# Optimization experiments

Measured on AMD Instinct MI355X. Metric: run time of the kernel, lower is better.

The kernel has to match this reference:

```python
import jax, jax.numpy as jnp
import numpy as np

N_NODES = 50000
N_EDGES = 800000
NODE_IN = 128
EDGE_IN = 16
HIDDEN = 128
OUT = 128


def setup_inputs() -> dict:
    key = jax.random.key(0)
    ks = jax.random.split(key, 8)
    x = jax.random.normal(ks[0], (N_NODES, NODE_IN), dtype=jnp.float32)
    edge_index = jax.random.randint(ks[1], (2, N_EDGES), 0, N_NODES, dtype=jnp.int64)
    edge_attr = jax.random.normal(ks[2], (N_EDGES, EDGE_IN), dtype=jnp.float32)
    # Linear weights stored as [in, out] (torch Linear weight is [out, in]); kaiming-ish scale
    s1 = 1.0 / np.sqrt(NODE_IN + EDGE_IN)
    s2 = 1.0 / np.sqrt(HIDDEN + EDGE_IN)
    W1 = jax.random.uniform(ks[3], (NODE_IN + EDGE_IN, HIDDEN), jnp.float32, -s1, s1)
    b1 = jnp.zeros((HIDDEN,), jnp.float32)
    W2 = jax.random.uniform(ks[4], (HIDDEN + EDGE_IN, OUT), jnp.float32, -s2, s2)
    b2 = jnp.zeros((OUT,), jnp.float32)
    return {"x": x, "edge_index": edge_index, "edge_attr": edge_attr,
            "W1": W1, "b1": b1, "W2": W2, "b2": b2}


def _edge_conv(x, src, dst, edge_attr, W, b, num_nodes):
    # message: lin(cat([x_j, edge_attr])) == x_j @ W_x + edge_attr @ W_e
    d = x.shape[1]
    Wx, We = W[:d], W[d:]
    msg = x[src] @ Wx + edge_attr @ We           # [E, out]
    aggr = jax.ops.segment_sum(msg, dst, num_segments=num_nodes)  # scatter-add
    return aggr + b


def reference(x, edge_index, edge_attr, W1, b1, W2, b2):
    src, dst = edge_index[0], edge_index[1]
    h = jax.nn.relu(_edge_conv(x, src, dst, edge_attr, W1, b1, N_NODES))
    return _edge_conv(h, src, dst, edge_attr, W2, b2, N_NODES)
```

## Files before the change

kernel.cpp:

```cpp
#include <hip/hip_runtime.h>

#define N_NODES 50000
#define N_EDGES 800000
#define F_NODE 128
#define F_EDGE 16

#define BUCK_SH 6
#define NBUCK ((N_NODES + 63) >> BUCK_SH)
#define NPART 8
#define CAP_PART 304
#define BCUR_STRIDE 16

#define CONV_BLOCKS ((N_NODES * 32 + 255) / 256)
#define SCAT_BLOCKS ((N_EDGES + 255) / 256)
#define NB128 ((N_NODES + 3) / 4)
#define NB16  ((N_NODES + 3) / 4)

__device__ __forceinline__ unsigned int bf16_rn(float f) {
    unsigned int u = __float_as_uint(f);
    unsigned int r = ((u >> 16) & 1u) + 0x7fffu;
    return (u + r) >> 16;
}
__device__ __forceinline__ unsigned int pack_bf16(float a, float b) {
    return bf16_rn(a) | (bf16_rn(b) << 16);
}
__device__ __forceinline__ float bf_lo(unsigned int u) { return __uint_as_float(u << 16); }
__device__ __forceinline__ float bf_hi(unsigned int u) { return __uint_as_float(u & 0xffff0000u); }

__global__ __launch_bounds__(256) void convert_and_scatter(
    const float4* __restrict__ x4, uint2* __restrict__ xb2,
    const int* __restrict__ src, const int* __restrict__ dst,
    int* __restrict__ bcur, unsigned long long* __restrict__ temp)
{
    if (blockIdx.x < CONV_BLOCKS) {
        int i = blockIdx.x * 256 + threadIdx.x;
        float4 v = x4[i];
        uint2 o;
        o.x = pack_bf16(v.x, v.y);
        o.y = pack_bf16(v.z, v.w);
        xb2[i] = o;
    } else {
        int e = (int)(blockIdx.x - CONV_BLOCKS) * 256 + threadIdx.x;
        if (e >= N_EDGES) return;
        int d = dst[e];
        int b = d >> BUCK_SH;
        int dl = d & 63;
        int cell = b * NPART + (blockIdx.x & (NPART - 1));
        int pos = atomicAdd(&bcur[cell * BCUR_STRIDE], 1);
        if (pos < CAP_PART)
            temp[(size_t)cell * CAP_PART + pos] =
                (unsigned long long)src[e] |
                ((unsigned long long)e  << 17) |
                ((unsigned long long)dl << 37);
    }
}

__global__ __launch_bounds__(1024) void cell_scan(const int* __restrict__ bcur,
                                                  int* __restrict__ bucket_base) {
    __shared__ int sh[1024];
    int t = threadIdx.x;
    int tot = 0;
    if (t < NBUCK) {
        #pragma unroll
        for (int p = 0; p < NPART; ++p) {
            int m = bcur[(t * NPART + p) * BCUR_STRIDE];
            tot += (m > CAP_PART ? CAP_PART : m);
        }
    }
    sh[t] = tot;
    __syncthreads();
    for (int off = 1; off < 1024; off <<= 1) {
        int v = (t >= off) ? sh[t - off] : 0;
        __syncthreads();
        sh[t] += v;
        __syncthreads();
    }
    if (t < NBUCK) bucket_base[t] = sh[t] - tot;
}

__global__ __launch_bounds__(256) void bucket_permute(
    const unsigned long long* __restrict__ temp,
    const int* __restrict__ bcur,
    const int* __restrict__ bucket_base,
    int* __restrict__ rs,
    int* __restrict__ csr_src, int* __restrict__ csr_eid)
{
    __shared__ int cnt[64];
    __shared__ int scn[64];
    __shared__ int cnt2[64];
    int b = blockIdx.x;
    int tid = threadIdx.x;
    int node0 = b << BUCK_SH;
    int nn = min(64, N_NODES - node0);
    if (tid < 64) { cnt[tid] = 0; cnt2[tid] = 0; }
    __syncthreads();
    int base = bucket_base[b];

    for (int part = 0; part < NPART; ++part) {
        int cell = b * NPART + part;
        int m = bcur[cell * BCUR_STRIDE];
        if (m > CAP_PART) m = CAP_PART;
        size_t tb = (size_t)cell * CAP_PART;
        for (int i = tid; i < m; i += 256) {
            int dl = (int)(temp[tb + i] >> 37);
            atomicAdd(&cnt[dl], 1);
        }
    }
    __syncthreads();

    if (tid < 64) scn[tid] = cnt[tid];
    __syncthreads();
    for (int o = 1; o < 64; o <<= 1) {
        int v = 0;
        if (tid < 64 && tid >= o) v = scn[tid - o];
        __syncthreads();
        if (tid < 64) scn[tid] += v;
        __syncthreads();
    }
    if (tid < nn) rs[node0 + tid] = base + scn[tid] - cnt[tid];
    if (b == NBUCK - 1 && tid == 0) rs[N_NODES] = base + scn[63];

    for (int part = 0; part < NPART; ++part) {
        int cell = b * NPART + part;
        int m = bcur[cell * BCUR_STRIDE];
        if (m > CAP_PART) m = CAP_PART;
        size_t tb = (size_t)cell * CAP_PART;
        for (int i = tid; i < m; i += 256) {
            unsigned long long v = temp[tb + i];
            int s  = (int)(v & 0x1FFFF);
            int ei = (int)((v >> 17) & 0xFFFFF);
            int dl = (int)(v >> 37);
            int pos = base + (scn[dl] - cnt[dl]) + atomicAdd(&cnt2[dl], 1);
            csr_src[pos] = s;
            csr_eid[pos] = ei;
        }
    }
}

__device__ __forceinline__ void agg128_body(const unsigned int* __restrict__ xb,
                                            const int* __restrict__ rs,
                                            const int* __restrict__ csr_src,
                                            float* __restrict__ xa,
                                            int bid) {
    int gid = bid * 256 + (int)threadIdx.x;
    int n = gid >> 6;
    int lane = threadIdx.x & 63;
    if (n >= N_NODES) return;
    int beg = rs[n], end = rs[n + 1];
    float a0 = 0.f, a1 = 0.f;
    int i = beg;
    for (; i + 8 <= end; i += 8) {
        int s[8];
        #pragma unroll
        for (int t = 0; t < 8; ++t) s[t] = csr_src[i + t];
        unsigned int u[8];
        #pragma unroll
        for (int t = 0; t < 8; ++t) u[t] = xb[(size_t)s[t] * 64 + lane];
        #pragma unroll
        for (int t = 0; t < 8; ++t) { a0 += bf_lo(u[t]); a1 += bf_hi(u[t]); }
    }
    for (; i + 4 <= end; i += 4) {
        int s[4];
        #pragma unroll
        for (int t = 0; t < 4; ++t) s[t] = csr_src[i + t];
        unsigned int u[4];
        #pragma unroll
        for (int t = 0; t < 4; ++t) u[t] = xb[(size_t)s[t] * 64 + lane];
        #pragma unroll
        for (int t = 0; t < 4; ++t) { a0 += bf_lo(u[t]); a1 += bf_hi(u[t]); }
    }
    for (; i < end; ++i) {
        unsigned int u = xb[(size_t)csr_src[i] * 64 + lane];
        a0 += bf_lo(u);
        a1 += bf_hi(u);
    }
    *(float2*)(xa + (size_t)n * F_NODE + lane * 2) = make_float2(a0, a1);
}

__device__ __forceinline__ void agg16_body(const float4* __restrict__ eattr4,
                                           const int* __restrict__ rs,
                                           const int* __restrict__ csr_eid,
                                           float* __restrict__ eagg,
                                           int bid) {
    int gid = bid * 256 + (int)threadIdx.x;
    int n = gid >> 6;
    int lane = threadIdx.x & 63;
    int sub = lane >> 2;
    int j4  = lane & 3;
    if (n >= N_NODES) return;
    int beg = rs[n], end = rs[n + 1];
    float4 acc = make_float4(0.f, 0.f, 0.f, 0.f);
    for (int i = beg + sub; i < end; i += 16) {
        int eid = csr_eid[i];
        float4 v = eattr4[(size_t)eid * 4 + j4];
        acc.x += v.x; acc.y += v.y; acc.z += v.z; acc.w += v.w;
    }
    #pragma unroll
    for (int m = 4; m <= 32; m <<= 1) {
        acc.x += __shfl_xor(acc.x, m, 64);
        acc.y += __shfl_xor(acc.y, m, 64);
        acc.z += __shfl_xor(acc.z, m, 64);
        acc.w += __shfl_xor(acc.w, m, 64);
    }
    if (sub == 0) *(float4*)(eagg + (size_t)n * F_EDGE + j4 * 4) = acc;
}

__global__ __launch_bounds__(256) void agg_combo(const unsigned int* __restrict__ xb,
                                                 const float4* __restrict__ eattr4,
                                                 const int* __restrict__ rs,
                                                 const int* __restrict__ csr_src,
                                                 const int* __restrict__ csr_eid,
                                                 float* __restrict__ xa,
                                                 float* __restrict__ eagg) {
    if (blockIdx.x < NB128)
        agg128_body(xb, rs, csr_src, xa, blockIdx.x);
    else
        agg16_body(eattr4, rs, csr_eid, eagg, blockIdx.x - NB128);
}

__global__ __launch_bounds__(256) void agg128_bf16(const unsigned int* __restrict__ xb,
                                                   const int* __restrict__ rs,
                                                   const int* __restrict__ csr_src,
                                                   float* __restrict__ xa) {
    agg128_body(xb, rs, csr_src, xa, blockIdx.x);
}

#define BM 64
#define BK 16
#define LDA (BM + 4)
#define LDB (128 + 4)

__global__ __launch_bounds__(256) void layer_gemm(
    const float* xa,
    const float* __restrict__ eagg,
    const float* __restrict__ W,
    const float* __restrict__ bias,
    float* out_f32,
    unsigned int* __restrict__ out_bf,
    int do_relu, int out_bf16)
{
    __shared__ float As[BK][LDA];
    __shared__ float Bs[BK][LDB];
    const int tid = threadIdx.x;
    const int bm = blockIdx.x * BM;

    const int tcol = (tid & 15) * 8;
    const int trow = (tid >> 4) * 4;

    const int lm = tid >> 2;
    const int lk = (tid & 3) * 4;
    const int bk = tid >> 4;
    const int bj = (tid & 15) * 8;

    const int row = bm + lm;
    const bool rowok = row < N_NODES;

    float acc[4][8];
    #pragma unroll
    for (int i = 0; i < 4; ++i)
        #pragma unroll
        for (int j = 0; j < 8; ++j) acc[i][j] = 0.f;

    for (int k0 = 0; k0 < 144; k0 += BK) {
        float4 av = make_float4(0.f, 0.f, 0.f, 0.f);
        if (rowok) {
            if (k0 < F_NODE)
                av = *(const float4*)(xa + (size_t)row * F_NODE + k0 + lk);
            else
                av = *(const float4*)(eagg + (size_t)row * F_EDGE + lk);
        }
        As[lk + 0][lm] = av.x;
        As[lk + 1][lm] = av.y;
        As[lk + 2][lm] = av.z;
        As[lk + 3][lm] = av.w;

        const float4 b0 = *(const float4*)(W + (size_t)(k0 + bk) * 128 + bj);
        const float4 b1 = *(const float4*)(W + (size_t)(k0 + bk) * 128 + bj + 4);
        *(float4*)(&Bs[bk][bj])     = b0;
        *(float4*)(&Bs[bk][bj + 4]) = b1;
        __syncthreads();

        #pragma unroll
        for (int k = 0; k < BK; ++k) {
            float a0 = As[k][trow + 0];
            float a1 = As[k][trow + 1];
            float a2 = As[k][trow + 2];
            float a3 = As[k][trow + 3];
            float bv[8];
            #pragma unroll
            for (int j = 0; j < 8; ++j) bv[j] = Bs[k][tcol + j];
            #pragma unroll
            for (int j = 0; j < 8; ++j) {
                acc[0][j] = fmaf(a0, bv[j], acc[0][j]);
                acc[1][j] = fmaf(a1, bv[j], acc[1][j]);
                acc[2][j] = fmaf(a2, bv[j], acc[2][j]);
                acc[3][j] = fmaf(a3, bv[j], acc[3][j]);
            }
        }
        __syncthreads();
    }

    float4 bb0 = *(const float4*)(bias + tcol);
    float4 bb1 = *(const float4*)(bias + tcol + 4);
    #pragma unroll
    for (int i = 0; i < 4; ++i) {
        int r = bm + trow + i;
        if (r >= N_NODES) break;
        float v[8];
        v[0] = acc[i][0] + bb0.x; v[1] = acc[i][1] + bb0.y;
        v[2] = acc[i][2] + bb0.z; v[3] = acc[i][3] + bb0.w;
        v[4] = acc[i][4] + bb1.x; v[5] = acc[i][5] + bb1.y;
        v[6] = acc[i][6] + bb1.z; v[7] = acc[i][7] + bb1.w;
        if (do_relu) {
            #pragma unroll
            for (int j = 0; j < 8; ++j) v[j] = fmaxf(v[j], 0.f);
        }
        if (out_bf16) {
            uint4 s;
            s.x = pack_bf16(v[0], v[1]);
            s.y = pack_bf16(v[2], v[3]);
            s.z = pack_bf16(v[4], v[5]);
            s.w = pack_bf16(v[6], v[7]);
            *(uint4*)(out_bf + (size_t)r * 64 + tcol / 2) = s;
        } else {
            *(float4*)(out_f32 + (size_t)r * 128 + tcol)     = make_float4(v[0], v[1], v[2], v[3]);
            *(float4*)(out_f32 + (size_t)r * 128 + tcol + 4) = make_float4(v[4], v[5], v[6], v[7]);
        }
    }
}

static inline char* align16(char* p) {
    return (char*)(((uintptr_t)p + 15) & ~(uintptr_t)15);
}

extern "C" void kernel_launch(void* const* d_in, const int* in_sizes, int n_in,
                              void* d_out, int out_size, void* d_ws, size_t ws_size,
                              hipStream_t stream) {
    const float* x     = (const float*)d_in[0];
    const int*   eidx  = (const int*)  d_in[1];
    const float* eattr = (const float*)d_in[2];
    const float* W1    = (const float*)d_in[3];
    const float* b1    = (const float*)d_in[4];
    const float* W2    = (const float*)d_in[5];
    const float* b2    = (const float*)d_in[6];
    float* out = (float*)d_out;

    const int* srcv = eidx;
    const int* dstv = eidx + N_EDGES;

    char* p = (char*)d_ws;
    unsigned int* xbhb = (unsigned int*)p;  p += (size_t)N_NODES * 64 * 4;
    float* eagg        = (float*)p;         p += (size_t)N_NODES * F_EDGE * 4;
    unsigned long long* temp = (unsigned long long*)p;
    p += (size_t)NBUCK * NPART * CAP_PART * 8;
    int* csr_src = (int*)p;                 p += (size_t)N_EDGES * 4;
    int* csr_eid = (int*)p;                 p += (size_t)N_EDGES * 4;
    int* rs      = (int*)p;                 p += (size_t)(N_NODES + 1) * 4;
    p = align16(p);
    int* bucket_base = (int*)p;             p += (size_t)NBUCK * 4;
    p = align16(p);
    int* bcur    = (int*)p;                 p += (size_t)NBUCK * NPART * BCUR_STRIDE * 4;

    float* xa = out;

    hipMemsetAsync(bcur, 0, (size_t)NBUCK * NPART * BCUR_STRIDE * 4, stream);

    convert_and_scatter<<<CONV_BLOCKS + SCAT_BLOCKS, 256, 0, stream>>>(
        (const float4*)x, (uint2*)xbhb, srcv, dstv, bcur, temp);

    cell_scan<<<1, 1024, 0, stream>>>(bcur, bucket_base);

    bucket_permute<<<NBUCK, 256, 0, stream>>>(temp, bcur, bucket_base, rs,
                                              csr_src, csr_eid);

    agg_combo<<<NB128 + NB16, 256, 0, stream>>>(
        xbhb, (const float4*)eattr, rs, csr_src, csr_eid, xa, eagg);

    layer_gemm<<<(N_NODES + BM - 1) / BM, 256, 0, stream>>>(
        xa, eagg, W1, b1, (float*)nullptr, xbhb, 1, 1);

    agg128_bf16<<<NB128, 256, 0, stream>>>(xbhb, rs, csr_src, xa);

    layer_gemm<<<(N_NODES + BM - 1) / BM, 256, 0, stream>>>(
        xa, eagg, W2, b2, out, (unsigned int*)nullptr, 0, 0);
}
```

Measured before the change: 317.5 us.

## Precompute per-node degree histogram during scatter, widen partitions, unroll gather by 16

```diff
diff --git a/kernel.cpp b/kernel.cpp
--- a/kernel.cpp
+++ b/kernel.cpp
@@ -7,8 +7,8 @@
 
 #define BUCK_SH 6
 #define NBUCK ((N_NODES + 63) >> BUCK_SH)
-#define NPART 8
-#define CAP_PART 304
+#define NPART 16
+#define CAP_PART 160
 #define BCUR_STRIDE 16
 
 #define CONV_BLOCKS ((N_NODES * 32 + 255) / 256)
@@ -30,7 +30,8 @@
 __global__ __launch_bounds__(256) void convert_and_scatter(
     const float4* __restrict__ x4, uint2* __restrict__ xb2,
     const int* __restrict__ src, const int* __restrict__ dst,
-    int* __restrict__ bcur, unsigned long long* __restrict__ temp)
+    int* __restrict__ bcur, int* __restrict__ hist,
+    unsigned long long* __restrict__ temp)
 {
     if (blockIdx.x < CONV_BLOCKS) {
         int i = blockIdx.x * 256 + threadIdx.x;
@@ -46,6 +47,7 @@
         int b = d >> BUCK_SH;
         int dl = d & 63;
         int cell = b * NPART + (blockIdx.x & (NPART - 1));
+        atomicAdd(&hist[d], 1);
         int pos = atomicAdd(&bcur[cell * BCUR_STRIDE], 1);
         if (pos < CAP_PART)
             temp[(size_t)cell * CAP_PART + pos] =
@@ -82,6 +84,7 @@
     const unsigned long long* __restrict__ temp,
     const int* __restrict__ bcur,
     const int* __restrict__ bucket_base,
+    const int* __restrict__ hist,
     int* __restrict__ rs,
     int* __restrict__ csr_src, int* __restrict__ csr_eid)
 {
@@ -92,21 +95,12 @@
     int tid = threadIdx.x;
     int node0 = b << BUCK_SH;
     int nn = min(64, N_NODES - node0);
-    if (tid < 64) { cnt[tid] = 0; cnt2[tid] = 0; }
+    if (tid < 64) {
+        cnt2[tid] = 0;
+        cnt[tid] = (tid < nn) ? hist[node0 + tid] : 0;
+    }
     __syncthreads();
     int base = bucket_base[b];
-
-    for (int part = 0; part < NPART; ++part) {
-        int cell = b * NPART + part;
-        int m = bcur[cell * BCUR_STRIDE];
-        if (m > CAP_PART) m = CAP_PART;
-        size_t tb = (size_t)cell * CAP_PART;
-        for (int i = tid; i < m; i += 256) {
-            int dl = (int)(temp[tb + i] >> 37);
-            atomicAdd(&cnt[dl], 1);
-        }
-    }
-    __syncthreads();
 
     if (tid < 64) scn[tid] = cnt[tid];
     __syncthreads();
@@ -149,6 +143,16 @@
     int beg = rs[n], end = rs[n + 1];
     float a0 = 0.f, a1 = 0.f;
     int i = beg;
+    for (; i + 16 <= end; i += 16) {
+        int s[16];
+        #pragma unroll
+        for (int t = 0; t < 16; ++t) s[t] = csr_src[i + t];
+        unsigned int u[16];
+        #pragma unroll
+        for (int t = 0; t < 16; ++t) u[t] = xb[(size_t)s[t] * 64 + lane];
+        #pragma unroll
+        for (int t = 0; t < 16; ++t) { a0 += bf_lo(u[t]); a1 += bf_hi(u[t]); }
+    }
     for (; i + 8 <= end; i += 8) {
         int s[8];
         #pragma unroll
@@ -360,17 +364,20 @@
     int* bucket_base = (int*)p;             p += (size_t)NBUCK * 4;
     p = align16(p);
     int* bcur    = (int*)p;                 p += (size_t)NBUCK * NPART * BCUR_STRIDE * 4;
+    int* hist    = (int*)p;                 p += (size_t)N_NODES * 4;
 
     float* xa = out;
 
-    hipMemsetAsync(bcur, 0, (size_t)NBUCK * NPART * BCUR_STRIDE * 4, stream);
+    hipMemsetAsync(bcur, 0,
+                   (size_t)NBUCK * NPART * BCUR_STRIDE * 4 + (size_t)N_NODES * 4,
+                   stream);
 
     convert_and_scatter<<<CONV_BLOCKS + SCAT_BLOCKS, 256, 0, stream>>>(
-        (const float4*)x, (uint2*)xbhb, srcv, dstv, bcur, temp);
+        (const float4*)x, (uint2*)xbhb, srcv, dstv, bcur, hist, temp);
 
     cell_scan<<<1, 1024, 0, stream>>>(bcur, bucket_base);
 
-    bucket_permute<<<NBUCK, 256, 0, stream>>>(temp, bcur, bucket_base, rs,
+    bucket_permute<<<NBUCK, 256, 0, stream>>>(temp, bcur, bucket_base, hist, rs,
                                               csr_src, csr_eid);
 
     agg_combo<<<NB128 + NB16, 256, 0, stream>>>(
```

New measurement: 360.3 us. 1.13x slower.

## Split bf16 node features into four column slabs for cache-local gathers

Applied to the files above, without the earlier changes.

```diff
diff --git a/kernel.cpp b/kernel.cpp
--- a/kernel.cpp
+++ b/kernel.cpp
@@ -13,8 +13,9 @@
 
 #define CONV_BLOCKS ((N_NODES * 32 + 255) / 256)
 #define SCAT_BLOCKS ((N_EDGES + 255) / 256)
-#define NB128 ((N_NODES + 3) / 4)
-#define NB16  ((N_NODES + 3) / 4)
+
+#define NBQ   (N_NODES / 4)
+#define NB16  (N_NODES / 4)
 
 __device__ __forceinline__ unsigned int bf16_rn(float f) {
     unsigned int u = __float_as_uint(f);
@@ -28,17 +29,20 @@
 __device__ __forceinline__ float bf_hi(unsigned int u) { return __uint_as_float(u & 0xffff0000u); }
 
 __global__ __launch_bounds__(256) void convert_and_scatter(
-    const float4* __restrict__ x4, uint2* __restrict__ xb2,
+    const float4* __restrict__ x4, uint2* __restrict__ xbq2,
     const int* __restrict__ src, const int* __restrict__ dst,
     int* __restrict__ bcur, unsigned long long* __restrict__ temp)
 {
     if (blockIdx.x < CONV_BLOCKS) {
         int i = blockIdx.x * 256 + threadIdx.x;
         float4 v = x4[i];
+        int n = i >> 5;
+        int c = i & 31;
+        int q = c >> 3;
         uint2 o;
         o.x = pack_bf16(v.x, v.y);
         o.y = pack_bf16(v.z, v.w);
-        xb2[i] = o;
+        xbq2[(size_t)(q * N_NODES + n) * 8 + (c & 7)] = o;
     } else {
         int e = (int)(blockIdx.x - CONV_BLOCKS) * 256 + threadIdx.x;
         if (e >= N_EDGES) return;
@@ -137,44 +141,63 @@
     }
 }
 
-__device__ __forceinline__ void agg128_body(const unsigned int* __restrict__ xb,
-                                            const int* __restrict__ rs,
-                                            const int* __restrict__ csr_src,
-                                            float* __restrict__ xa,
-                                            int bid) {
-    int gid = bid * 256 + (int)threadIdx.x;
-    int n = gid >> 6;
+__device__ __forceinline__ void aggq_body(const unsigned int* __restrict__ xbq,
+                                          const int* __restrict__ rs,
+                                          const int* __restrict__ csr_src,
+                                          float* __restrict__ xa,
+                                          int bid) {
+    int q   = bid / NBQ;
+    int nb  = bid - q * NBQ;
+    int wid = threadIdx.x >> 6;
+    int n   = nb * 4 + wid;
     int lane = threadIdx.x & 63;
+    int sub  = lane >> 4;
+    int f    = lane & 15;
     if (n >= N_NODES) return;
+    const unsigned int* pool = xbq + (size_t)q * N_NODES * 16;
     int beg = rs[n], end = rs[n + 1];
     float a0 = 0.f, a1 = 0.f;
-    int i = beg;
-    for (; i + 8 <= end; i += 8) {
-        int s[8];
-        #pragma unroll
-        for (int t = 0; t < 8; ++t) s[t] = csr_src[i + t];
-        unsigned int u[8];
-        #pragma unroll
-        for (int t = 0; t < 8; ++t) u[t] = xb[(size_t)s[t] * 64 + lane];
+    int base = beg;
+    for (; base + 32 <= end; base += 32) {
+        int s[8]; unsigned int u[8];
+        #pragma unroll
+        for (int t = 0; t < 8; ++t) s[t] = csr_src[base + sub + 4 * t];
+        #pragma unroll
+        for (int t = 0; t < 8; ++t) u[t] = pool[(size_t)s[t] * 16 + f];
         #pragma unroll
         for (int t = 0; t < 8; ++t) { a0 += bf_lo(u[t]); a1 += bf_hi(u[t]); }
     }
-    for (; i + 4 <= end; i += 4) {
-        int s[4];
-        #pragma unroll
-        for (int t = 0; t < 4; ++t) s[t] = csr_src[i + t];
-        unsigned int u[4];
-        #pragma unroll
-        for (int t = 0; t < 4; ++t) u[t] = xb[(size_t)s[t] * 64 + lane];
+    for (; base + 16 <= end; base += 16) {
+        int s[4]; unsigned int u[4];
+        #pragma unroll
+        for (int t = 0; t < 4; ++t) s[t] = csr_src[base + sub + 4 * t];
+        #pragma unroll
+        for (int t = 0; t < 4; ++t) u[t] = pool[(size_t)s[t] * 16 + f];
         #pragma unroll
         for (int t = 0; t < 4; ++t) { a0 += bf_lo(u[t]); a1 += bf_hi(u[t]); }
     }
-    for (; i < end; ++i) {
-        unsigned int u = xb[(size_t)csr_src[i] * 64 + lane];
-        a0 += bf_lo(u);
-        a1 += bf_hi(u);
-    }
-    *(float2*)(xa + (size_t)n * F_NODE + lane * 2) = make_float2(a0, a1);
+    for (; base + 8 <= end; base += 8) {
+        int s[2]; unsigned int u[2];
+        #pragma unroll
+        for (int t = 0; t < 2; ++t) s[t] = csr_src[base + sub + 4 * t];
+        #pragma unroll
+        for (int t = 0; t < 2; ++t) u[t] = pool[(size_t)s[t] * 16 + f];
+        #pragma unroll
+        for (int t = 0; t < 2; ++t) { a0 += bf_lo(u[t]); a1 += bf_hi(u[t]); }
+    }
+    for (; base + 4 <= end; base += 4) {
+        unsigned int u = pool[(size_t)csr_src[base + sub] * 16 + f];
+        a0 += bf_lo(u); a1 += bf_hi(u);
+    }
+    int rem = end - base;
+    if (sub < rem) {
+        unsigned int u = pool[(size_t)csr_src[base + sub] * 16 + f];
+        a0 += bf_lo(u); a1 += bf_hi(u);
+    }
+    a0 += __shfl_xor(a0, 16, 64); a0 += __shfl_xor(a0, 32, 64);
+    a1 += __shfl_xor(a1, 16, 64); a1 += __shfl_xor(a1, 32, 64);
+    if (sub == 0)
+        *(float2*)(xa + (size_t)n * F_NODE + q * 32 + f * 2) = make_float2(a0, a1);
 }
 
 __device__ __forceinline__ void agg16_body(const float4* __restrict__ eattr4,
@@ -205,24 +228,24 @@
     if (sub == 0) *(float4*)(eagg + (size_t)n * F_EDGE + j4 * 4) = acc;
 }
 
-__global__ __launch_bounds__(256) void agg_combo(const unsigned int* __restrict__ xb,
+__global__ __launch_bounds__(256) void agg_combo(const unsigned int* __restrict__ xbq,
                                                  const float4* __restrict__ eattr4,
                                                  const int* __restrict__ rs,
                                                  const int* __restrict__ csr_src,
                                                  const int* __restrict__ csr_eid,
                                                  float* __restrict__ xa,
                                                  float* __restrict__ eagg) {
-    if (blockIdx.x < NB128)
-        agg128_body(xb, rs, csr_src, xa, blockIdx.x);
+    if (blockIdx.x < NB16)
+        agg16_body(eattr4, rs, csr_eid, eagg, blockIdx.x);
     else
-        agg16_body(eattr4, rs, csr_eid, eagg, blockIdx.x - NB128);
-}
-
-__global__ __launch_bounds__(256) void agg128_bf16(const unsigned int* __restrict__ xb,
-                                                   const int* __restrict__ rs,
-                                                   const int* __restrict__ csr_src,
-                                                   float* __restrict__ xa) {
-    agg128_body(xb, rs, csr_src, xa, blockIdx.x);
+        aggq_body(xbq, rs, csr_src, xa, blockIdx.x - NB16);
+}
+
+__global__ __launch_bounds__(256) void aggq_bf16(const unsigned int* __restrict__ xbq,
+                                                 const int* __restrict__ rs,
+                                                 const int* __restrict__ csr_src,
+                                                 float* __restrict__ xa) {
+    aggq_body(xbq, rs, csr_src, xa, blockIdx.x);
 }
 
 #define BM 64
@@ -321,7 +344,9 @@
             s.y = pack_bf16(v[2], v[3]);
             s.z = pack_bf16(v[4], v[5]);
             s.w = pack_bf16(v[6], v[7]);
-            *(uint4*)(out_bf + (size_t)r * 64 + tcol / 2) = s;
+            int q  = tcol >> 5;
+            int jj = (tcol & 31) >> 1;
+            *(uint4*)(out_bf + (size_t)(q * N_NODES + r) * 16 + jj) = s;
         } else {
             *(float4*)(out_f32 + (size_t)r * 128 + tcol)     = make_float4(v[0], v[1], v[2], v[3]);
             *(float4*)(out_f32 + (size_t)r * 128 + tcol + 4) = make_float4(v[4], v[5], v[6], v[7]);
@@ -373,13 +398,13 @@
     bucket_permute<<<NBUCK, 256, 0, stream>>>(temp, bcur, bucket_base, rs,
                                               csr_src, csr_eid);
 
-    agg_combo<<<NB128 + NB16, 256, 0, stream>>>(
+    agg_combo<<<NB16 + 4 * NBQ, 256, 0, stream>>>(
         xbhb, (const float4*)eattr, rs, csr_src, csr_eid, xa, eagg);
 
     layer_gemm<<<(N_NODES + BM - 1) / BM, 256, 0, stream>>>(
         xa, eagg, W1, b1, (float*)nullptr, xbhb, 1, 1);
 
-    agg128_bf16<<<NB128, 256, 0, stream>>>(xbhb, rs, csr_src, xa);
+    aggq_bf16<<<4 * NBQ, 256, 0, stream>>>(xbhb, rs, csr_src, xa);
 
     layer_gemm<<<(N_NODES + BM - 1) / BM, 256, 0, stream>>>(
         xa, eagg, W2, b2, out, (unsigned int*)nullptr, 0, 0);
```

Result: slower. 382.5 us (+20.5%).
